# Kernel tuning notes

Hardware: AMD Instinct MI355X
Metric: run time of the kernel (lower is better)

The kernel has to match this reference:

```python
import jax, jax.numpy as jnp
import numpy as np

D_MODEL = 1024
NUM_HEADS = 16
HEAD_DIM = D_MODEL // NUM_HEADS
HIDDEN = 4096
EPS = 1e-5


def setup_inputs() -> dict:
    key = jax.random.key(0)
    ks = jax.random.split(key, 10)
    s = 0.02
    return {
        "x": jax.random.normal(ks[0], (2, 2048, D_MODEL), dtype=jnp.float32),
        # attention projection weights stored as (in, out): y = x @ W
        "wq": jax.random.normal(ks[1], (D_MODEL, D_MODEL), dtype=jnp.float32) * s,
        "wk": jax.random.normal(ks[2], (D_MODEL, D_MODEL), dtype=jnp.float32) * s,
        "wv": jax.random.normal(ks[3], (D_MODEL, D_MODEL), dtype=jnp.float32) * s,
        "wo": jax.random.normal(ks[4], (D_MODEL, D_MODEL), dtype=jnp.float32) * s,
        # FFN
        "w1": jax.random.normal(ks[5], (D_MODEL, HIDDEN), dtype=jnp.float32) * s,
        "b1": jnp.zeros((HIDDEN,), dtype=jnp.float32),
        "w2": jax.random.normal(ks[6], (HIDDEN, D_MODEL), dtype=jnp.float32) * s,
        "b2": jnp.zeros((D_MODEL,), dtype=jnp.float32),
        # LayerNorms
        "g1": jnp.ones((D_MODEL,), dtype=jnp.float32),
        "be1": jnp.zeros((D_MODEL,), dtype=jnp.float32),
        "g2": jnp.ones((D_MODEL,), dtype=jnp.float32),
        "be2": jnp.zeros((D_MODEL,), dtype=jnp.float32),
    }


def _layernorm(x, g, b):
    mu = jnp.mean(x, axis=-1, keepdims=True)
    var = jnp.mean(jnp.square(x - mu), axis=-1, keepdims=True)
    return (x - mu) * jax.lax.rsqrt(var + EPS) * g + b


def _attention(x, wq, wk, wv, wo):
    B, S, D = x.shape
    q = (x @ wq).reshape(B, S, NUM_HEADS, HEAD_DIM)
    k = (x @ wk).reshape(B, S, NUM_HEADS, HEAD_DIM)
    v = (x @ wv).reshape(B, S, NUM_HEADS, HEAD_DIM)
    scores = jnp.einsum("bqhd,bkhd->bhqk", q, k) / jnp.sqrt(
        jnp.float32(HEAD_DIM)
    )
    causal = jnp.tril(jnp.ones((S, S), dtype=bool))
    scores = jnp.where(causal, scores, -jnp.inf)
    probs = jax.nn.softmax(scores, axis=-1)
    out = jnp.einsum("bhqk,bkhd->bqhd", probs, v).reshape(B, S, D)
    return out @ wo


def _ffn(x, w1, b1, w2, b2):
    return jax.nn.relu(x @ w1 + b1) @ w2 + b2


def reference(x, wq, wk, wv, wo, w1, b1, w2, b2, g1, be1, g2, be2):
    x = x + _attention(_layernorm(x, g1, be1), wq, wk, wv, wo)
    x = x + _ffn(_layernorm(x, g2, be2), w1, b1, w2, b2)
    return x
```

## Files before the change

kernel.cpp:

```cpp
#include <hip/hip_runtime.h>
#include <stdint.h>

typedef unsigned short bf16u;
typedef __attribute__((ext_vector_type(8))) __bf16 bf16x8;
typedef __attribute__((ext_vector_type(4))) float f32x4;
typedef __attribute__((ext_vector_type(4))) unsigned short u16x4;
typedef __attribute__((ext_vector_type(8))) unsigned short u16x8;

typedef __attribute__((address_space(1))) void gvoid_t;
typedef __attribute__((address_space(3))) void lvoid_t;

#define SEQ 2048
#define DM 1024
#define MN22 4194304
#define SCL 0.18033688f

__device__ __forceinline__ bf16u f2bf(float f) {
  union { float f; uint32_t u; } v; v.f = f;
  uint32_t u = v.u + 0x7fffu + ((v.u >> 16) & 1u);
  return (bf16u)(u >> 16);
}

__device__ __forceinline__ bf16u f2bf_hw(float f) {
  union { __bf16 h; bf16u u; } v; v.h = (__bf16)f; return v.u;
}

__device__ __forceinline__ float bf2f(bf16u b) {
  union { uint32_t u; float f; } v; v.u = (uint32_t)b << 16; return v.f;
}

__device__ __forceinline__ float exp2_hw(float x) {
  return __builtin_amdgcn_exp2f(x);
}

__device__ __forceinline__ void async_copy16(const bf16u* g, const bf16u* l) {
  __builtin_amdgcn_global_load_lds((gvoid_t*)(uintptr_t)g,
                                   (lvoid_t*)(uint32_t)(uintptr_t)l,
                                   16, 0, 0);
}

#define VM_WAIT(n) asm volatile("s_waitcnt vmcnt(" #n ")" ::: "memory")
#define LGKM0()    asm volatile("s_waitcnt lgkmcnt(0)" ::: "memory")
#define BARRIER()  asm volatile("s_barrier" ::: "memory")

__global__ __launch_bounds__(256) void ln_kernel(const float* __restrict__ x,
                                                 const float* __restrict__ g,
                                                 const float* __restrict__ be,
                                                 bf16u* __restrict__ out) {
  const int row = blockIdx.x;
  const int t = threadIdx.x;
  const float4 v = ((const float4*)(x + (size_t)row * DM))[t];
  float s  = v.x + v.y + v.z + v.w;
  float ss = v.x * v.x + v.y * v.y + v.z * v.z + v.w * v.w;
#pragma unroll
  for (int m = 1; m < 64; m <<= 1) {
    s  += __shfl_xor(s, m, 64);
    ss += __shfl_xor(ss, m, 64);
  }
  __shared__ float red[2][4];
  const int wv = t >> 6, ln = t & 63;
  if (ln == 0) { red[0][wv] = s; red[1][wv] = ss; }
  __syncthreads();
  s  = red[0][0] + red[0][1] + red[0][2] + red[0][3];
  ss = red[1][0] + red[1][1] + red[1][2] + red[1][3];
  const float mu = s * (1.0f / DM);
  const float var = ss * (1.0f / DM) - mu * mu;
  const float rstd = rsqrtf(var + 1e-5f);
  const float4 gg = ((const float4*)g)[t];
  const float4 bb = ((const float4*)be)[t];
  u16x4 o;
  o[0] = f2bf((v.x - mu) * rstd * gg.x + bb.x);
  o[1] = f2bf((v.y - mu) * rstd * gg.y + bb.y);
  o[2] = f2bf((v.z - mu) * rstd * gg.z + bb.z);
  o[3] = f2bf((v.w - mu) * rstd * gg.w + bb.w);
  *(u16x4*)(out + (size_t)row * DM + t * 4) = o;
}

__global__ __launch_bounds__(256) void prep_kernel(
    const float* __restrict__ x, const float* __restrict__ g,
    const float* __restrict__ be, bf16u* __restrict__ lnout,
    const float* __restrict__ wq, const float* __restrict__ wk,
    const float* __restrict__ wv_, const float* __restrict__ wo,
    bf16u* __restrict__ wqkv_t,
    const float* __restrict__ w1, bf16u* __restrict__ w1_t,
    const float* __restrict__ w2, bf16u* __restrict__ w2_t) {
  const int bid = blockIdx.x;
  const int t = threadIdx.x;
  if (bid < 4096) {
    const int row = bid;
    const float4 v = ((const float4*)(x + (size_t)row * DM))[t];
    float s  = v.x + v.y + v.z + v.w;
    float ss = v.x * v.x + v.y * v.y + v.z * v.z + v.w * v.w;
#pragma unroll
    for (int m = 1; m < 64; m <<= 1) {
      s  += __shfl_xor(s, m, 64);
      ss += __shfl_xor(ss, m, 64);
    }
    __shared__ float red[2][4];
    const int wv = t >> 6, ln = t & 63;
    if (ln == 0) { red[0][wv] = s; red[1][wv] = ss; }
    __syncthreads();
    s  = red[0][0] + red[0][1] + red[0][2] + red[0][3];
    ss = red[1][0] + red[1][1] + red[1][2] + red[1][3];
    const float mu = s * (1.0f / DM);
    const float var = ss * (1.0f / DM) - mu * mu;
    const float rstd = rsqrtf(var + 1e-5f);
    const float4 gg = ((const float4*)g)[t];
    const float4 bb = ((const float4*)be)[t];
    u16x4 o;
    o[0] = f2bf((v.x - mu) * rstd * gg.x + bb.x);
    o[1] = f2bf((v.y - mu) * rstd * gg.y + bb.y);
    o[2] = f2bf((v.z - mu) * rstd * gg.z + bb.z);
    o[3] = f2bf((v.w - mu) * rstd * gg.w + bb.w);
    *(u16x4*)(lnout + (size_t)row * DM + t * 4) = o;
    return;
  }
  __shared__ float tile[32][33];
  const int tx = t & 31, ty = t >> 5;
  const float* in; bf16u* o; int R, C, c0, r0;
  if (bid < 8192) {
    const int idx = bid - 4096;
    const int mat = idx >> 10, rem = idx & 1023;
    const float* srcs[4] = {wq, wk, wv_, wo};
    in = srcs[mat]; o = wqkv_t + (size_t)mat * 1024 * 1024;
    R = 1024; C = 1024;
    c0 = (rem & 31) * 32; r0 = (rem >> 5) * 32;
  } else if (bid < 12288) {
    const int idx = bid - 8192;
    in = w1; o = w1_t; R = 1024; C = 4096;
    c0 = (idx & 127) * 32; r0 = (idx >> 7) * 32;
  } else {
    const int idx = bid - 12288;
    in = w2; o = w2_t; R = 4096; C = 1024;
    c0 = (idx & 31) * 32; r0 = (idx >> 5) * 32;
  }
#pragma unroll
  for (int i = 0; i < 4; ++i)
    tile[ty + i * 8][tx] = in[(size_t)(r0 + ty + i * 8) * C + c0 + tx];
  __syncthreads();
#pragma unroll
  for (int i = 0; i < 4; ++i)
    o[(size_t)(c0 + ty + i * 8) * R + r0 + tx] = f2bf(tile[tx][ty + i * 8]);
}

__global__ __launch_bounds__(256) void reduce3(const bf16u* __restrict__ p01,
                                               const bf16u* __restrict__ p2,
                                               const float* __restrict__ bias,
                                               float* __restrict__ out) {
  const size_t i8 = ((size_t)blockIdx.x * 256 + threadIdx.x) * 8;
  const int col0 = (int)(i8 & 1023);
  const u16x8 a = *(const u16x8*)(p01 + i8);
  const u16x8 b = *(const u16x8*)(p01 + MN22 + i8);
  const u16x8 c = *(const u16x8*)(p2 + i8);
  const float4 o0 = *(const float4*)(out + i8);
  const float4 o1 = *(const float4*)(out + i8 + 4);
  const float4 b0 = *(const float4*)(bias + col0);
  const float4 b1 = *(const float4*)(bias + col0 + 4);
  float r[8];
#pragma unroll
  for (int j = 0; j < 8; ++j) r[j] = bf2f(a[j]) + bf2f(b[j]) + bf2f(c[j]);
  float4 w0, w1;
  w0.x = o0.x + r[0] + b0.x; w0.y = o0.y + r[1] + b0.y;
  w0.z = o0.z + r[2] + b0.z; w0.w = o0.w + r[3] + b0.w;
  w1.x = o1.x + r[4] + b1.x; w1.y = o1.y + r[5] + b1.y;
  w1.z = o1.z + r[6] + b1.z; w1.w = o1.w + r[7] + b1.w;
  *(float4*)(out + i8) = w0;
  *(float4*)(out + i8 + 4) = w1;
}

__global__ __launch_bounds__(512, 1) void gemm256(
    const bf16u* __restrict__ A, const bf16u* __restrict__ Bt,
    int M, int N, int K,
    const float* __restrict__ bias, bf16u* __restrict__ outB,
    bf16u* __restrict__ vt, int mode) {
  __shared__ bf16u sh[2][32768];
  const int t = threadIdx.x;
  const int ln = t & 63;
  const int wv = t >> 6;
  const int col16 = ln & 15, quad = ln >> 4;
  const int wm = wv >> 2, wn = wv & 3;

  const int nsplit = (mode == 6) ? 3 : 1;
  const int nbx = N >> 8;
  const int nwg = nbx * (M >> 8) * nsplit;
  const int cpx = nwg >> 3;
  const int bid = blockIdx.x;
  const int swz = (bid & 7) * cpx + (bid >> 3);
  const int tile = swz / nsplit, split = swz - tile * nsplit;
  const int m0 = (tile / nbx) << 8, n0 = (tile % nbx) << 8;
  const int tsteps = K >> 6;
  const int kbeg = (split * tsteps) / nsplit;
  const int nt = ((split + 1) * tsteps) / nsplit - kbeg;
  const size_t koff = (size_t)kbeg << 6;

  const bf16u* gsrc[4][2];
  int doff[4][2];
#pragma unroll
  for (int j = 0; j < 2; ++j) {
    const int c = t + (j << 9);
    const int lr = c >> 3, slot = (c & 7) ^ (lr & 7);
    const int ra = (lr & 63) + ((lr >> 6) << 7);
    const int rb = (lr & 31) + ((lr >> 5) << 6);
    gsrc[0][j] = A  + (size_t)(m0 + ra) * K + koff + slot * 8;
    gsrc[3][j] = A  + (size_t)(m0 + ra + 64) * K + koff + slot * 8;
    gsrc[1][j] = Bt + (size_t)(n0 + rb) * K + koff + slot * 8;
    gsrc[2][j] = Bt + (size_t)(n0 + rb + 32) * K + koff + slot * 8;
    doff[0][j] = c * 8;
    doff[3][j] = 8192 + c * 8;
    doff[1][j] = 16384 + c * 8;
    doff[2][j] = 24576 + c * 8;
  }

  const int sx = col16 & 7;
  int aoffs[4][2], boffs[2][2];
#pragma unroll
  for (int i = 0; i < 4; ++i)
#pragma unroll
    for (int kc = 0; kc < 2; ++kc)
      aoffs[i][kc] = (wm * 64 + i * 16 + col16) * 64 + (((kc << 2) + quad) ^ sx) * 8;
#pragma unroll
  for (int i = 0; i < 2; ++i)
#pragma unroll
    for (int kc = 0; kc < 2; ++kc)
      boffs[i][kc] = 16384 + (wn * 32 + i * 16 + col16) * 64 + (((kc << 2) + quad) ^ sx) * 8;

  f32x4 acc[8][4] = {};
  bf16x8 Af[4][2], Bf[4][2];

  auto stage = [&](int s, int b) {
#pragma unroll
    for (int j = 0; j < 2; ++j) {
      async_copy16(gsrc[s][j], &sh[b][doff[s][j]]);
      gsrc[s][j] += 64;
    }
  };
  auto readA = [&](int b, int mh) {
#pragma unroll
    for (int i = 0; i < 4; ++i)
#pragma unroll
      for (int kc = 0; kc < 2; ++kc)
        Af[i][kc] = *(const bf16x8*)(&sh[b][mh * 8192 + aoffs[i][kc]]);
  };
  auto readB = [&](int b, int nh) {
#pragma unroll
    for (int i = 0; i < 2; ++i)
#pragma unroll
      for (int kc = 0; kc < 2; ++kc)
        Bf[nh * 2 + i][kc] = *(const bf16x8*)(&sh[b][nh * 8192 + boffs[i][kc]]);
  };
  auto mfmaQ = [&](int mh, int nh) {
#pragma unroll
    for (int kc = 0; kc < 2; ++kc)
#pragma unroll
      for (int mi = 0; mi < 4; ++mi)
#pragma unroll
        for (int nl = 0; nl < 2; ++nl)
          acc[mh * 4 + mi][nh * 2 + nl] = __builtin_amdgcn_mfma_f32_16x16x32_bf16(
              Af[mi][kc], Bf[nh * 2 + nl][kc], acc[mh * 4 + mi][nh * 2 + nl], 0, 0, 0);
  };

  stage(0, 0); stage(1, 0); stage(2, 0); stage(3, 0);
  VM_WAIT(4);
  BARRIER();

  int bsel = 0;
  for (int kt = 0; kt < nt - 1; ++kt, bsel ^= 1) {
    const int bn = bsel ^ 1;
    readA(bsel, 0); readB(bsel, 0);
    stage(0, bn);
    BARRIER(); LGKM0();
    __builtin_amdgcn_s_setprio(1); mfmaQ(0, 0); __builtin_amdgcn_s_setprio(0);
    VM_WAIT(4); BARRIER();
    readB(bsel, 1);
    stage(1, bn);
    BARRIER(); LGKM0();
    __builtin_amdgcn_s_setprio(1); mfmaQ(0, 1); __builtin_amdgcn_s_setprio(0);
    VM_WAIT(4); BARRIER();
    readA(bsel, 1);
    stage(2, bn);
    BARRIER(); LGKM0();
    __builtin_amdgcn_s_setprio(1); mfmaQ(1, 0); __builtin_amdgcn_s_setprio(0);
    BARRIER();
    stage(3, bn);
    __builtin_amdgcn_s_setprio(1); mfmaQ(1, 1); __builtin_amdgcn_s_setprio(0);
    VM_WAIT(4); BARRIER();
  }
  readA(bsel, 0); readB(bsel, 0);
  BARRIER(); LGKM0();
  __builtin_amdgcn_s_setprio(1); mfmaQ(0, 0); __builtin_amdgcn_s_setprio(0);
  VM_WAIT(2); BARRIER();
  readB(bsel, 1);
  BARRIER(); LGKM0();
  __builtin_amdgcn_s_setprio(1); mfmaQ(0, 1); __builtin_amdgcn_s_setprio(0);
  VM_WAIT(0); BARRIER();
  readA(bsel, 1);
  LGKM0();
  __builtin_amdgcn_s_setprio(1); mfmaQ(1, 0); mfmaQ(1, 1); __builtin_amdgcn_s_setprio(0);

  if (mode == 6) {
    bf16u* pb = (split < 2) ? outB + (size_t)split * MN22 : vt;
#pragma unroll
    for (int mi = 0; mi < 8; ++mi) {
#pragma unroll
      for (int n = 0; n < 4; ++n) {
        const int col = n0 + wn * 64 + n * 16 + col16;
#pragma unroll
        for (int r = 0; r < 4; ++r) {
          const int row = m0 + wm * 128 + mi * 16 + quad * 4 + r;
          pb[(size_t)row * N + col] = f2bf(acc[mi][n][r]);
        }
      }
    }
    return;
  }
  if (mode == 5 && n0 >= 2048) {
#pragma unroll
    for (int mi = 0; mi < 8; ++mi) {
#pragma unroll
      for (int n = 0; n < 4; ++n) {
        const int col = n0 + wn * 64 + n * 16 + col16;
        const int hh = (col - 2048) >> 6, d = (col - 2048) & 63;
        const int row_base = m0 + wm * 128 + mi * 16 + quad * 4;
        const int bb = row_base >> 11, s = row_base & 2047;
        u16x4 o;
#pragma unroll
        for (int r = 0; r < 4; ++r) o[r] = f2bf(acc[mi][n][r]);
        *(u16x4*)(vt + (size_t)((bb * 16 + hh) * 64 + d) * SEQ + s) = o;
      }
    }
    return;
  }
  const float qscale = (mode == 5 && n0 < 1024) ? SCL : 1.0f;
  float bv[4];
  if (mode == 1) {
#pragma unroll
    for (int n = 0; n < 4; ++n) bv[n] = bias[n0 + wn * 64 + n * 16 + col16];
  }
#pragma unroll
  for (int mi = 0; mi < 8; ++mi) {
#pragma unroll
    for (int n = 0; n < 4; ++n) {
      const int col = n0 + wn * 64 + n * 16 + col16;
#pragma unroll
      for (int r = 0; r < 4; ++r) {
        const int row = m0 + wm * 128 + mi * 16 + quad * 4 + r;
        float v = acc[mi][n][r];
        if (mode == 1) v = fmaxf(v + bv[n], 0.0f);
        outB[(size_t)row * N + col] = f2bf(v * qscale);
      }
    }
  }
}

__global__ __launch_bounds__(256, 3) void gemm_bt64(
    const bf16u* __restrict__ A, const bf16u* __restrict__ Bt,
    int M, int N, int K,
    const float* __restrict__ bias, const float* __restrict__ resid,
    bf16u* __restrict__ outB, float* __restrict__ outF, int mode) {
  __shared__ bf16u As0[64 * 64], As1[64 * 64];
  __shared__ bf16u Bs0[128 * 64], Bs1[128 * 64];
  const int t = threadIdx.x;
  const int ln = t & 63;
  const int wv = t >> 6;
  const int col16 = ln & 15, quad = ln >> 4;

  const int nbx = gridDim.x;
  const int nwg = nbx * gridDim.y;
  const int cpx = nwg >> 3;
  const int flat = blockIdx.y * nbx + blockIdx.x;
  const int swz = (flat & 7) * cpx + (flat >> 3);
  const int m0 = (swz / nbx) * 64, n0 = (swz % nbx) * 128;

  const bf16u* gA[2];
  const bf16u* gB[4];
#pragma unroll
  for (int j = 0; j < 2; ++j) {
    const int c = t + 256 * j, row = c >> 3, slot = (c & 7) ^ (row & 7);
    gA[j] = A + (size_t)(m0 + row) * K + slot * 8;
  }
#pragma unroll
  for (int j = 0; j < 4; ++j) {
    const int c = t + 256 * j, row = c >> 3, slot = (c & 7) ^ (row & 7);
    gB[j] = Bt + (size_t)(n0 + row) * K + slot * 8;
  }

  f32x4 acc[4][2] = {};

  auto stage = [&](bf16u* dA, bf16u* dB) {
#pragma unroll
    for (int j = 0; j < 2; ++j) {
      async_copy16(gA[j], dA + (size_t)(t + 256 * j) * 8);
      gA[j] += 64;
    }
#pragma unroll
    for (int j = 0; j < 4; ++j) {
      async_copy16(gB[j], dB + (size_t)(t + 256 * j) * 8);
      gB[j] += 64;
    }
  };
  auto compute = [&](const bf16u* sA, const bf16u* sB) {
    bf16x8 af[4][2], bfv[2][2];
#pragma unroll
    for (int mi = 0; mi < 4; ++mi) {
      const int row = mi * 16 + col16;
#pragma unroll
      for (int kc = 0; kc < 2; ++kc)
        af[mi][kc] = *(const bf16x8*)(sA + row * 64 + (((kc << 2) + quad) ^ (row & 7)) * 8);
    }
#pragma unroll
    for (int ni = 0; ni < 2; ++ni) {
      const int row = wv * 32 + ni * 16 + col16;
#pragma unroll
      for (int kc = 0; kc < 2; ++kc)
        bfv[ni][kc] = *(const bf16x8*)(sB + row * 64 + (((kc << 2) + quad) ^ (row & 7)) * 8);
    }
#pragma unroll
    for (int kc = 0; kc < 2; ++kc)
#pragma unroll
      for (int mi = 0; mi < 4; ++mi)
#pragma unroll
        for (int ni = 0; ni < 2; ++ni)
          acc[mi][ni] = __builtin_amdgcn_mfma_f32_16x16x32_bf16(af[mi][kc], bfv[ni][kc],
                                                                acc[mi][ni], 0, 0, 0);
  };

  const int niter = K >> 6;
  stage(As0, Bs0);
  for (int k = 0; k < niter; k += 2) {
    stage(As1, Bs1);
    VM_WAIT(6);
    BARRIER();
    compute(As0, Bs0);
    BARRIER();
    if (k + 2 < niter) {
      stage(As0, Bs0);
      VM_WAIT(6);
    } else {
      VM_WAIT(0);
    }
    BARRIER();
    compute(As1, Bs1);
    BARRIER();
  }

#pragma unroll
  for (int mi = 0; mi < 4; ++mi) {
#pragma unroll
    for (int ni = 0; ni < 2; ++ni) {
      const int col = n0 + wv * 32 + ni * 16 + col16;
#pragma unroll
      for (int r = 0; r < 4; ++r) {
        const int row = m0 + mi * 16 + quad * 4 + r;
        float v = acc[mi][ni][r];
        if (mode == 1 || mode == 3) v += bias[col];
        if (mode == 1) v = fmaxf(v, 0.0f);
        if (mode >= 2) {
          outF[(size_t)row * N + col] = v + resid[(size_t)row * N + col];
        } else {
          outB[(size_t)row * N + col] = f2bf(v);
        }
      }
    }
  }
}

#define PST 132
__global__ __launch_bounds__(256, 3) void attn_kernel(const bf16u* __restrict__ qkv,
                                                      const bf16u* __restrict__ vt,
                                                      bf16u* __restrict__ out) {
  __shared__ bf16u Ks[128 * 64];
  __shared__ bf16u Vts[2 * 64 * 64];
  __shared__ bf16u pbuf[4][16 * PST];
  __shared__ float lred[4][16];
  const int t = threadIdx.x;
  const int wv = t >> 6, ln = t & 63;
  const int col = ln & 15, quad = ln >> 4;
  const int bh = blockIdx.x, b = bh >> 4, h = bh & 15;
  const int strip = 31 - blockIdx.y;
  const int q0 = strip * 64;
  const int qw = q0 + wv * 16;
  const int qmax = qw + 15;
  const int ntiles = (q0 >> 7) + 1;

  int krow[4], kslot[4], vrow[4], vsub[4], vslot[4];
  const bf16u *kl[4], *vl[4];
#pragma unroll
  for (int j = 0; j < 4; ++j) {
    const int c = t + 256 * j;
    krow[j] = c >> 3; kslot[j] = (c & 7) ^ (krow[j] & 7);
    const int rem = c & 511;
    vsub[j] = c >> 9; vrow[j] = rem >> 3; vslot[j] = (rem & 7) ^ (vrow[j] & 7);
    kl[j] = Ks + (size_t)c * 8;
    vl[j] = Vts + (size_t)c * 8;
  }

  auto stageK = [&](int kb) {
    const int kbase = kb * 128;
#pragma unroll
    for (int j = 0; j < 4; ++j)
      async_copy16(qkv + (size_t)(b * SEQ + kbase + krow[j]) * 3072 + 1024 + h * 64 + kslot[j] * 8, kl[j]);
  };
  auto stageV = [&](int kb) {
    const int kbase = kb * 128;
#pragma unroll
    for (int j = 0; j < 4; ++j)
      async_copy16(vt + (size_t)(bh * 64 + vrow[j]) * SEQ + kbase + vsub[j] * 64 + vslot[j] * 8, vl[j]);
  };

  bf16x8 qf0, qf1;
  {
    const size_t qoff = (size_t)(b * SEQ + qw + col) * 3072 + h * 64 + quad * 8;
    qf0 = *(const bf16x8*)(qkv + qoff);
    qf1 = *(const bf16x8*)(qkv + qoff + 32);
  }
  f32x4 po[4] = {};
  float ll[4] = {};

  stageK(0);
  stageV(0);
  VM_WAIT(4);
  BARRIER();

  for (int kb = 0; kb < ntiles; ++kb) {
    const int kbase = kb * 128;
    if (kb < ntiles - 1) {
      f32x4 sc[8];
#pragma unroll
      for (int n = 0; n < 8; ++n) {
        const int kr = n * 16 + col;
        const bf16x8 k0 = *(const bf16x8*)(Ks + kr * 64 + (quad ^ (kr & 7)) * 8);
        const bf16x8 k1 = *(const bf16x8*)(Ks + kr * 64 + ((4 + quad) ^ (kr & 7)) * 8);
        f32x4 z = {};
        z = __builtin_amdgcn_mfma_f32_16x16x32_bf16(qf0, k0, z, 0, 0, 0);
        sc[n] = __builtin_amdgcn_mfma_f32_16x16x32_bf16(qf1, k1, z, 0, 0, 0);
      }
#pragma unroll
      for (int r = 0; r < 4; ++r) {
#pragma unroll
        for (int n = 0; n < 8; ++n) {
          const float e = exp2_hw(sc[n][r]);
          ll[r] += e;
          pbuf[wv][(quad * 4 + r) * PST + n * 16 + col] = f2bf_hw(e);
        }
      }
    } else {
      f32x4 sc[8];
      bool act[8];
#pragma unroll
      for (int n = 0; n < 8; ++n) {
        act[n] = (kbase + n * 16) <= qmax;
        if (act[n]) {
          const int kr = n * 16 + col;
          const bf16x8 k0 = *(const bf16x8*)(Ks + kr * 64 + (quad ^ (kr & 7)) * 8);
          const bf16x8 k1 = *(const bf16x8*)(Ks + kr * 64 + ((4 + quad) ^ (kr & 7)) * 8);
          f32x4 z = {};
          z = __builtin_amdgcn_mfma_f32_16x16x32_bf16(qf0, k0, z, 0, 0, 0);
          sc[n] = __builtin_amdgcn_mfma_f32_16x16x32_bf16(qf1, k1, z, 0, 0, 0);
        }
      }
#pragma unroll
      for (int r = 0; r < 4; ++r) {
        const int q = qw + quad * 4 + r;
#pragma unroll
        for (int n = 0; n < 8; ++n) {
          float e = 0.0f;
          if (act[n]) {
            float v = sc[n][r];
            v = (kbase + n * 16 + col <= q) ? v : -1e30f;
            e = exp2_hw(v);
          }
          ll[r] += e;
          pbuf[wv][(quad * 4 + r) * PST + n * 16 + col] = f2bf_hw(e);
        }
      }
    }
    LGKM0();
    bf16x8 pa[4];
#pragma unroll
    for (int kc = 0; kc < 4; ++kc)
      pa[kc] = *(const bf16x8*)(&pbuf[wv][col * PST + kc * 32 + quad * 8]);
    VM_WAIT(0);
    BARRIER();
    if (kb + 1 < ntiles) stageK(kb + 1);
    if (kb < ntiles - 1) {
#pragma unroll
      for (int n = 0; n < 4; ++n) {
        const int vr = n * 16 + col;
#pragma unroll
        for (int kc = 0; kc < 4; ++kc) {
          const bf16x8 vfr = *(const bf16x8*)(Vts + (kc >> 1) * 4096 + vr * 64 +
                                              (((kc & 1) * 4 + quad) ^ (vr & 7)) * 8);
          po[n] = __builtin_amdgcn_mfma_f32_16x16x32_bf16(vfr, pa[kc], po[n], 0, 0, 0);
        }
      }
    } else {
#pragma unroll
      for (int n = 0; n < 4; ++n) {
        const int vr = n * 16 + col;
#pragma unroll
        for (int kc = 0; kc < 4; ++kc)
          if (kbase + kc * 32 <= qmax) {
            const bf16x8 vfr = *(const bf16x8*)(Vts + (kc >> 1) * 4096 + vr * 64 +
                                                (((kc & 1) * 4 + quad) ^ (vr & 7)) * 8);
            po[n] = __builtin_amdgcn_mfma_f32_16x16x32_bf16(vfr, pa[kc], po[n], 0, 0, 0);
          }
      }
    }
    if (kb + 1 < ntiles) {
      LGKM0();
      BARRIER();
      stageV(kb + 1);
      VM_WAIT(4);
      BARRIER();
    }
  }

#pragma unroll
  for (int m = 1; m < 16; m <<= 1)
#pragma unroll
    for (int r = 0; r < 4; ++r) ll[r] += __shfl_xor(ll[r], m, 64);
  if (col == 0) {
#pragma unroll
    for (int r = 0; r < 4; ++r) lred[wv][quad * 4 + r] = ll[r];
  }
  LGKM0();
  const float inv = 1.0f / lred[wv][col];
#pragma unroll
  for (int n = 0; n < 4; ++n) {
    u16x4 o;
#pragma unroll
    for (int r = 0; r < 4; ++r) o[r] = f2bf(po[n][r] * inv);
    *(u16x4*)(out + (size_t)(b * SEQ + qw + col) * DM + h * 64 + n * 16 + quad * 4) = o;
  }
}

extern "C" void kernel_launch(void* const* d_in, const int* in_sizes, int n_in,
                              void* d_out, int out_size, void* d_ws, size_t ws_size,
                              hipStream_t stream) {
  const float* x   = (const float*)d_in[0];
  const float* wq  = (const float*)d_in[1];
  const float* wk  = (const float*)d_in[2];
  const float* wvv = (const float*)d_in[3];
  const float* wo  = (const float*)d_in[4];
  const float* w1  = (const float*)d_in[5];
  const float* b1  = (const float*)d_in[6];
  const float* w2  = (const float*)d_in[7];
  const float* b2  = (const float*)d_in[8];
  const float* g1  = (const float*)d_in[9];
  const float* be1 = (const float*)d_in[10];
  const float* g2  = (const float*)d_in[11];
  const float* be2 = (const float*)d_in[12];
  float* out = (float*)d_out;

  char* ws = (char*)d_ws;
  bf16u* wqkv_t = (bf16u*)(ws);
  bf16u* wo_t   = (bf16u*)(ws +  6291456);
  bf16u* w1_t   = (bf16u*)(ws +  8388608);
  bf16u* w2_t   = (bf16u*)(ws + 16777216);
  bf16u* lnbuf  = (bf16u*)(ws + 25165824);
  bf16u* qkv    = (bf16u*)(ws + 33554432);
  bf16u* vtb    = (bf16u*)(ws + 58720256);
  bf16u* h1     = (bf16u*)(ws + 33554432);
  bf16u* attn   = lnbuf;
  bf16u* p01 = (bf16u*)(ws);
  bf16u* p2  = (bf16u*)(ws + 25165824);

  prep_kernel<<<16384, 256, 0, stream>>>(x, g1, be1, lnbuf,
                                         wq, wk, wvv, wo, wqkv_t,
                                         w1, w1_t, w2, w2_t);
  gemm256<<<192, 512, 0, stream>>>(lnbuf, wqkv_t, 4096, 3072, 1024,
                                   nullptr, qkv, vtb, 5);
  attn_kernel<<<dim3(32, 32), 256, 0, stream>>>(qkv, vtb, attn);
  gemm_bt64<<<dim3(8, 64), 256, 0, stream>>>(attn, wo_t, 4096, 1024, 1024,
                                             nullptr, x, nullptr, out, 2);
  ln_kernel<<<4096, 256, 0, stream>>>(out, g2, be2, lnbuf);
  gemm256<<<256, 512, 0, stream>>>(lnbuf, w1_t, 4096, 4096, 1024,
                                   b1, h1, nullptr, 1);
  gemm256<<<192, 512, 0, stream>>>(h1, w2_t, 4096, 1024, 4096,
                                   nullptr, p01, p2, 6);
  reduce3<<<2048, 256, 0, stream>>>(p01, p2, b2, out);
}
```

Before: 316.8 us.

## Shrink GEMM tiles to 128x128 with 4 waves, raise MFMA priority in attention

The bf16 GEMM kernel moves from 256x256 tiles with 8 waves to 128x128 tiles with 4 waves, two workgroups per CU, and half the LDS. The LDS swizzle and fragment offsets are recomputed, and grid sizes grow fourfold. The goal is better CU fill (256 CUs vs 192/256 tiles) and occupancy, at the cost of lower per-tile reuse and more global traffic. Separately, the attention kernel wraps its MFMA loops in s_setprio to favour matrix issue.

After: 318.4 us. Within noise of the previous version (+0.5%).

```diff
diff --git a/kernel.cpp b/kernel.cpp
--- a/kernel.cpp
+++ b/kernel.cpp
@@ -168,26 +168,26 @@
   *(float4*)(out + i8 + 4) = w1;
 }
 
-__global__ __launch_bounds__(512, 1) void gemm256(
+__global__ __launch_bounds__(256, 2) void gemm256(
     const bf16u* __restrict__ A, const bf16u* __restrict__ Bt,
     int M, int N, int K,
     const float* __restrict__ bias, bf16u* __restrict__ outB,
     bf16u* __restrict__ vt, int mode) {
-  __shared__ bf16u sh[2][32768];
+  __shared__ bf16u sh[2][16384];
   const int t = threadIdx.x;
   const int ln = t & 63;
   const int wv = t >> 6;
   const int col16 = ln & 15, quad = ln >> 4;
-  const int wm = wv >> 2, wn = wv & 3;
+  const int wm = wv >> 1, wn = wv & 1;
 
   const int nsplit = (mode == 6) ? 3 : 1;
-  const int nbx = N >> 8;
-  const int nwg = nbx * (M >> 8) * nsplit;
+  const int nbx = N >> 7;
+  const int nwg = nbx * (M >> 7) * nsplit;
   const int cpx = nwg >> 3;
   const int bid = blockIdx.x;
   const int swz = (bid & 7) * cpx + (bid >> 3);
   const int tile = swz / nsplit, split = swz - tile * nsplit;
-  const int m0 = (tile / nbx) << 8, n0 = (tile % nbx) << 8;
+  const int m0 = (tile / nbx) << 7, n0 = (tile % nbx) << 7;
   const int tsteps = K >> 6;
   const int kbeg = (split * tsteps) / nsplit;
   const int nt = ((split + 1) * tsteps) / nsplit - kbeg;
@@ -197,35 +197,34 @@
   int doff[4][2];
 #pragma unroll
   for (int j = 0; j < 2; ++j) {
-    const int c = t + (j << 9);
+    const int c = t + (j << 8);
     const int lr = c >> 3, slot = (c & 7) ^ (lr & 7);
-    const int ra = (lr & 63) + ((lr >> 6) << 7);
-    const int rb = (lr & 31) + ((lr >> 5) << 6);
-    gsrc[0][j] = A  + (size_t)(m0 + ra) * K + koff + slot * 8;
-    gsrc[3][j] = A  + (size_t)(m0 + ra + 64) * K + koff + slot * 8;
-    gsrc[1][j] = Bt + (size_t)(n0 + rb) * K + koff + slot * 8;
-    gsrc[2][j] = Bt + (size_t)(n0 + rb + 32) * K + koff + slot * 8;
+    const int rq = (lr & 31) + ((lr >> 5) << 6);
+    gsrc[0][j] = A  + (size_t)(m0 + rq) * K + koff + slot * 8;
+    gsrc[3][j] = A  + (size_t)(m0 + rq + 32) * K + koff + slot * 8;
+    gsrc[1][j] = Bt + (size_t)(n0 + rq) * K + koff + slot * 8;
+    gsrc[2][j] = Bt + (size_t)(n0 + rq + 32) * K + koff + slot * 8;
     doff[0][j] = c * 8;
-    doff[3][j] = 8192 + c * 8;
-    doff[1][j] = 16384 + c * 8;
-    doff[2][j] = 24576 + c * 8;
-  }
-
-  const int sx = col16 & 7;
-  int aoffs[4][2], boffs[2][2];
+    doff[3][j] = 4096 + c * 8;
+    doff[1][j] = 8192 + c * 8;
+    doff[2][j] = 12288 + c * 8;
+  }
+
+  int aoffs[4][2], boffs[4][2];
 #pragma unroll
   for (int i = 0; i < 4; ++i)
 #pragma unroll
-    for (int kc = 0; kc < 2; ++kc)
-      aoffs[i][kc] = (wm * 64 + i * 16 + col16) * 64 + (((kc << 2) + quad) ^ sx) * 8;
-#pragma unroll
-  for (int i = 0; i < 2; ++i)
-#pragma unroll
-    for (int kc = 0; kc < 2; ++kc)
-      boffs[i][kc] = 16384 + (wn * 32 + i * 16 + col16) * 64 + (((kc << 2) + quad) ^ sx) * 8;
-
-  f32x4 acc[8][4] = {};
-  bf16x8 Af[4][2], Bf[4][2];
+    for (int kc = 0; kc < 2; ++kc) {
+      const int ra = wm * 64 + i * 16 + col16;
+      const int la = ((ra >> 5) & 1) * 4096 + (((ra & 31) + ((ra >> 6) << 5)) << 6);
+      aoffs[i][kc] = la + (((kc << 2) + quad) ^ (ra & 7)) * 8;
+      const int rb = wn * 64 + i * 16 + col16;
+      const int lb = ((rb >> 5) & 1) * 4096 + (((rb & 31) + ((rb >> 6) << 5)) << 6);
+      boffs[i][kc] = 8192 + lb + (((kc << 2) + quad) ^ (rb & 7)) * 8;
+    }
+
+  f32x4 acc[4][4] = {};
+  bf16x8 Af[2][2], Bf[4][2];
 
   auto stage = [&](int s, int b) {
 #pragma unroll
@@ -236,27 +235,27 @@
   };
   auto readA = [&](int b, int mh) {
 #pragma unroll
-    for (int i = 0; i < 4; ++i)
+    for (int i = 0; i < 2; ++i)
 #pragma unroll
       for (int kc = 0; kc < 2; ++kc)
-        Af[i][kc] = *(const bf16x8*)(&sh[b][mh * 8192 + aoffs[i][kc]]);
+        Af[i][kc] = *(const bf16x8*)(&sh[b][aoffs[mh * 2 + i][kc]]);
   };
   auto readB = [&](int b, int nh) {
 #pragma unroll
     for (int i = 0; i < 2; ++i)
 #pragma unroll
       for (int kc = 0; kc < 2; ++kc)
-        Bf[nh * 2 + i][kc] = *(const bf16x8*)(&sh[b][nh * 8192 + boffs[i][kc]]);
+        Bf[nh * 2 + i][kc] = *(const bf16x8*)(&sh[b][boffs[nh * 2 + i][kc]]);
   };
   auto mfmaQ = [&](int mh, int nh) {
 #pragma unroll
     for (int kc = 0; kc < 2; ++kc)
 #pragma unroll
-      for (int mi = 0; mi < 4; ++mi)
+      for (int mi = 0; mi < 2; ++mi)
 #pragma unroll
         for (int nl = 0; nl < 2; ++nl)
-          acc[mh * 4 + mi][nh * 2 + nl] = __builtin_amdgcn_mfma_f32_16x16x32_bf16(
-              Af[mi][kc], Bf[nh * 2 + nl][kc], acc[mh * 4 + mi][nh * 2 + nl], 0, 0, 0);
+          acc[mh * 2 + mi][nh * 2 + nl] = __builtin_amdgcn_mfma_f32_16x16x32_bf16(
+              Af[mi][kc], Bf[nh * 2 + nl][kc], acc[mh * 2 + mi][nh * 2 + nl], 0, 0, 0);
   };
 
   stage(0, 0); stage(1, 0); stage(2, 0); stage(3, 0);
@@ -300,13 +299,13 @@
   if (mode == 6) {
     bf16u* pb = (split < 2) ? outB + (size_t)split * MN22 : vt;
 #pragma unroll
-    for (int mi = 0; mi < 8; ++mi) {
+    for (int mi = 0; mi < 4; ++mi) {
 #pragma unroll
       for (int n = 0; n < 4; ++n) {
         const int col = n0 + wn * 64 + n * 16 + col16;
 #pragma unroll
         for (int r = 0; r < 4; ++r) {
-          const int row = m0 + wm * 128 + mi * 16 + quad * 4 + r;
+          const int row = m0 + wm * 64 + mi * 16 + quad * 4 + r;
           pb[(size_t)row * N + col] = f2bf(acc[mi][n][r]);
         }
       }
@@ -315,12 +314,12 @@
   }
   if (mode == 5 && n0 >= 2048) {
 #pragma unroll
-    for (int mi = 0; mi < 8; ++mi) {
+    for (int mi = 0; mi < 4; ++mi) {
 #pragma unroll
       for (int n = 0; n < 4; ++n) {
         const int col = n0 + wn * 64 + n * 16 + col16;
         const int hh = (col - 2048) >> 6, d = (col - 2048) & 63;
-        const int row_base = m0 + wm * 128 + mi * 16 + quad * 4;
+        const int row_base = m0 + wm * 64 + mi * 16 + quad * 4;
         const int bb = row_base >> 11, s = row_base & 2047;
         u16x4 o;
 #pragma unroll
@@ -337,13 +336,13 @@
     for (int n = 0; n < 4; ++n) bv[n] = bias[n0 + wn * 64 + n * 16 + col16];
   }
 #pragma unroll
-  for (int mi = 0; mi < 8; ++mi) {
+  for (int mi = 0; mi < 4; ++mi) {
 #pragma unroll
     for (int n = 0; n < 4; ++n) {
       const int col = n0 + wn * 64 + n * 16 + col16;
 #pragma unroll
       for (int r = 0; r < 4; ++r) {
-        const int row = m0 + wm * 128 + mi * 16 + quad * 4 + r;
+        const int row = m0 + wm * 64 + mi * 16 + quad * 4 + r;
         float v = acc[mi][n][r];
         if (mode == 1) v = fmaxf(v + bv[n], 0.0f);
         outB[(size_t)row * N + col] = f2bf(v * qscale);
@@ -525,6 +524,7 @@
     const int kbase = kb * 128;
     if (kb < ntiles - 1) {
       f32x4 sc[8];
+      __builtin_amdgcn_s_setprio(1);
 #pragma unroll
       for (int n = 0; n < 8; ++n) {
         const int kr = n * 16 + col;
@@ -534,6 +534,7 @@
         z = __builtin_amdgcn_mfma_f32_16x16x32_bf16(qf0, k0, z, 0, 0, 0);
         sc[n] = __builtin_amdgcn_mfma_f32_16x16x32_bf16(qf1, k1, z, 0, 0, 0);
       }
+      __builtin_amdgcn_s_setprio(0);
 #pragma unroll
       for (int r = 0; r < 4; ++r) {
 #pragma unroll
@@ -546,6 +547,7 @@
     } else {
       f32x4 sc[8];
       bool act[8];
+      __builtin_amdgcn_s_setprio(1);
 #pragma unroll
       for (int n = 0; n < 8; ++n) {
         act[n] = (kbase + n * 16) <= qmax;
@@ -558,6 +560,7 @@
           sc[n] = __builtin_amdgcn_mfma_f32_16x16x32_bf16(qf1, k1, z, 0, 0, 0);
         }
       }
+      __builtin_amdgcn_s_setprio(0);
 #pragma unroll
       for (int r = 0; r < 4; ++r) {
         const int q = qw + quad * 4 + r;
@@ -583,6 +586,7 @@
     BARRIER();
     if (kb + 1 < ntiles) stageK(kb + 1);
     if (kb < ntiles - 1) {
+      __builtin_amdgcn_s_setprio(1);
 #pragma unroll
       for (int n = 0; n < 4; ++n) {
         const int vr = n * 16 + col;
@@ -593,7 +597,9 @@
           po[n] = __builtin_amdgcn_mfma_f32_16x16x32_bf16(vfr, pa[kc], po[n], 0, 0, 0);
         }
       }
+      __builtin_amdgcn_s_setprio(0);
     } else {
+      __builtin_amdgcn_s_setprio(1);
 #pragma unroll
       for (int n = 0; n < 4; ++n) {
         const int vr = n * 16 + col;
@@ -605,6 +611,7 @@
             po[n] = __builtin_amdgcn_mfma_f32_16x16x32_bf16(vfr, pa[kc], po[n], 0, 0, 0);
           }
       }
+      __builtin_amdgcn_s_setprio(0);
     }
     if (kb + 1 < ntiles) {
       LGKM0();
@@ -668,15 +675,15 @@
   prep_kernel<<<16384, 256, 0, stream>>>(x, g1, be1, lnbuf,
                                          wq, wk, wvv, wo, wqkv_t,
                                          w1, w1_t, w2, w2_t);
-  gemm256<<<192, 512, 0, stream>>>(lnbuf, wqkv_t, 4096, 3072, 1024,
+  gemm256<<<768, 256, 0, stream>>>(lnbuf, wqkv_t, 4096, 3072, 1024,
                                    nullptr, qkv, vtb, 5);
   attn_kernel<<<dim3(32, 32), 256, 0, stream>>>(qkv, vtb, attn);
   gemm_bt64<<<dim3(8, 64), 256, 0, stream>>>(attn, wo_t, 4096, 1024, 1024,
                                              nullptr, x, nullptr, out, 2);
   ln_kernel<<<4096, 256, 0, stream>>>(out, g2, be2, lnbuf);
-  gemm256<<<256, 512, 0, stream>>>(lnbuf, w1_t, 4096, 4096, 1024,
-                                   b1, h1, nullptr, 1);
-  gemm256<<<192, 512, 0, stream>>>(h1, w2_t, 4096, 1024, 4096,
+  gemm256<<<1024, 256, 0, stream>>>(lnbuf, w1_t, 4096, 4096, 1024,
+                                    b1, h1, nullptr, 1);
+  gemm256<<<768, 256, 0, stream>>>(h1, w2_t, 4096, 1024, 4096,
                                    nullptr, p01, p2, 6);
   reduce3<<<2048, 256, 0, stream>>>(p01, p2, b2, out);
 }
```
